# Kernel tuning notes

Hardware: AMD Instinct MI355X
Metric: run time of the kernel (lower is better)

## Reference

```python
import jax, jax.numpy as jnp
import numpy as np

N, S, E = 50000, 16, 400000
D, EDIM = 128, 64
H, K = 4, 32          # n_head, per-head output_dim
NMP, DEPTH = 2, 2


def attn_agg(x, neigh, Wq, Wk, Wv):
    # x: [n, D], neigh: [n, s, D], W*: [H, D, K]
    q = jnp.einsum('nd,hdk->nhk', x, Wq)
    k = jnp.einsum('nsd,hdk->nshk', neigh, Wk)
    v = jnp.einsum('nsd,hdk->nshk', neigh, Wv)
    scale = jnp.asarray(1.0 / np.sqrt(K), x.dtype)
    scores = jnp.einsum('nhk,nshk->nhs', q, k) * scale
    attn = jax.nn.softmax(scores, axis=-1)
    out = jax.nn.elu(jnp.einsum('nhs,nshk->nhk', attn, v))  # activation per head
    return out.reshape(out.shape[0], H * K)                  # concat heads


def setup_inputs():
    key = jax.random.key(0)
    ks = jax.random.split(key, 14)
    sD, sE = 1.0 / np.sqrt(D), 1.0 / np.sqrt(EDIM)
    return {
        'feats': jax.random.normal(ks[0], (N, D), jnp.float32),
        'node_emb': jax.random.normal(ks[1], (N, D), jnp.float32) * 0.02,
        'Wprep': jax.random.normal(ks[2], (D, D), jnp.float32) * sD,
        'edge_emb': jax.random.normal(ks[3], (NMP, E, EDIM), jnp.float32),
        'Wedgeprep': jax.random.normal(ks[4], (NMP, EDIM, D), jnp.float32) * sE,
        'Wq_e': jax.random.normal(ks[5], (NMP, DEPTH, H, D, K), jnp.float32) * sD,
        'Wk_e': jax.random.normal(ks[6], (NMP, DEPTH, H, D, K), jnp.float32) * sD,
        'Wv_e': jax.random.normal(ks[7], (NMP, DEPTH, H, D, K), jnp.float32) * sD,
        'Wq_n': jax.random.normal(ks[8], (NMP, DEPTH, H, D, K), jnp.float32) * sD,
        'Wk_n': jax.random.normal(ks[9], (NMP, DEPTH, H, D, K), jnp.float32) * sD,
        'Wv_n': jax.random.normal(ks[10], (NMP, DEPTH, H, D, K), jnp.float32) * sD,
        'node2edge_idx': jax.random.randint(ks[11], (NMP, N, S), 0, E, jnp.int32),
        'edge_node_adj': jax.random.randint(ks[12], (NMP, E, 2), 0, N, jnp.int32),
    }


def reference(feats, node_emb, Wprep, edge_emb, Wedgeprep,
              Wq_e, Wk_e, Wv_e, Wq_n, Wk_n, Wv_n,
              node2edge_idx, edge_node_adj):
    outputs = []
    for mp in range(NMP):
        f = jax.lax.stop_gradient(feats)           # feats[all_ids].detach()
        dummy_feats = node_emb                      # prep layer_idx=0 (id embedding)
        all_feats = f @ Wprep                       # prep layer_idx=1
        all_edges = edge_emb[mp] @ Wedgeprep[mp]    # edge_prep[mp], shuffle=False
        skip = []
        for l in range(DEPTH):
            # --- edge update: gather 2 endpoint node feats per edge ---
            en = all_feats[edge_node_adj[mp]]       # [E, 2, D]
            next_edges = attn_agg(all_edges, en, Wq_e[mp, l], Wk_e[mp, l], Wv_e[mp, l])
            # --- node update: gather S incident edge feats per node (OLD edges) ---
            x = dummy_feats if l == 0 else all_feats
            ne = all_edges[node2edge_idx[mp]]       # [N, S, D]
            next_feats = attn_agg(x, ne, Wq_n[mp, l], Wk_n[mp, l], Wv_n[mp, l])
            skip.append(next_feats)
            all_feats, all_edges = next_feats, next_edges
        outputs.append(jnp.concatenate(skip, axis=-1))  # [N, DEPTH*H*K]
    return jnp.stack(outputs, axis=0)                   # [NMP, N, DEPTH*H*K]
```

## Files before the change

kernel.cpp:

```cpp
#include <hip/hip_runtime.h>

#define N_NODES 50000
#define S_NEI 16
#define E_EDGES 400000
#define DDIM 128
#define EDIMC 64
#define NMPC 2
#define DEPTHC 2

typedef __attribute__((ext_vector_type(8))) short short8v;
typedef __attribute__((ext_vector_type(4))) float float4v;

__device__ __forceinline__ unsigned short f2bf(float f) {
  unsigned int u = __float_as_uint(f);
  unsigned int r = (u + 0x7fffu + ((u >> 16) & 1u)) >> 16;
  return (unsigned short)r;
}
__device__ __forceinline__ float bf2f(unsigned short h) { return __uint_as_float((unsigned int)h << 16); }
__device__ __forceinline__ float bflo(unsigned int u) { return __uint_as_float(u << 16); }
__device__ __forceinline__ float bfhi(unsigned int u) { return __uint_as_float(u & 0xffff0000u); }

__global__ void build_wt(const float* __restrict__ Wprep, const float* __restrict__ Wedgeprep,
                         const float* __restrict__ Wq_e, const float* __restrict__ Wk_e,
                         const float* __restrict__ Wv_e, const float* __restrict__ Wq_n,
                         const float* __restrict__ Wk_n, const float* __restrict__ Wv_n,
                         unsigned short* __restrict__ WT) {
  int idx = blockIdx.x * 256 + threadIdx.x;
  if (idx >= 27 * 16384) return;
  int slot = idx >> 14, r = idx & 16383;
  float v = 0.f;
  if (slot < 24) {
    int ml = slot / 6, mat = slot % 6;
    int c = r >> 7, d = r & 127;
    int h = c >> 5, kk = c & 31;
    const float* W = (mat == 0) ? Wk_e : (mat == 1) ? Wv_e : (mat == 2) ? Wq_n
                   : (mat == 3) ? Wq_e : (mat == 4) ? Wk_n : Wv_n;
    v = W[(((size_t)ml * 4 + h) * 128 + d) * 32 + kk];
  } else if (slot == 24) {
    int c = r >> 7, d = r & 127;
    v = Wprep[d * 128 + c];
  } else {
    int mp = slot - 25;
    int c = r >> 6, k = r & 63;
    if (c < 128) v = Wedgeprep[((size_t)mp * 64 + k) * 128 + c];
  }
  WT[idx] = f2bf(v);
}

template<int KDIM, int NW, bool ASPLIT>
__global__ __launch_bounds__(256, 3)
void proj(const unsigned short* __restrict__ Xbf, const float* __restrict__ Xf,
          const unsigned short* __restrict__ WT,
          unsigned short* __restrict__ Y0, unsigned short* __restrict__ Y1,
          unsigned short* __restrict__ Y2, int rs0, int rs1, int rs2, int M) {
  constexpr int NKK  = KDIM / 32;
  constexpr int CHPR = KDIM / 8;
  constexpr int SWZ  = CHPR - 1;
  __shared__ unsigned short Wl[128 * KDIM];
  const int tid  = threadIdx.x;
  const int lane = tid & 63;
  const int wv   = tid >> 6;
  const int l15  = lane & 15, lg = lane >> 4;
  const long m0  = (long)blockIdx.x * 128 + wv * 32;

  short8v xb[2][NKK];
  #pragma unroll
  for (int rf = 0; rf < 2; ++rf) {
    long row = m0 + rf * 16 + l15; if (row >= M) row = M - 1;
    #pragma unroll
    for (int kk = 0; kk < NKK; ++kk) {
      const int k0 = kk * 32 + lg * 8;
      if (ASPLIT) {
        const float* p = Xf + row * KDIM + k0;
        float4v a0 = *(const float4v*)p;
        float4v a1 = *(const float4v*)(p + 4);
        #pragma unroll
        for (int j = 0; j < 8; ++j) {
          float x = (j < 4) ? a0[j] : a1[j - 4];
          xb[rf][kk][j] = (short)f2bf(x);
        }
      } else {
        xb[rf][kk] = *(const short8v*)(Xbf + row * KDIM + k0);
      }
    }
  }

  unsigned short* Ys[3] = {Y0, Y1, Y2};
  const int rsv[3] = {rs0, rs1, rs2};
  #pragma unroll
  for (int w = 0; w < NW; ++w) {
    if (w) __syncthreads();
    {
      const uint4* src = (const uint4*)(WT + (size_t)w * 16384);
      #pragma unroll
      for (int i = 0; i < CHPR / 2; ++i) {
        int ci = i * 256 + tid;
        int row = ci / CHPR, ch = ci & SWZ;
        uint4 v = src[ci];
        *(uint4*)((char*)Wl + row * (KDIM * 2) + ((ch ^ (row & SWZ)) << 4)) = v;
      }
    }
    __syncthreads();

    float4v acc[8][2];
    #pragma unroll
    for (int cf = 0; cf < 8; ++cf)
      #pragma unroll
      for (int rf = 0; rf < 2; ++rf) acc[cf][rf] = (float4v)0.f;

    #pragma unroll
    for (int kk = 0; kk < NKK; ++kk) {
      #pragma unroll
      for (int cf = 0; cf < 8; ++cf) {
        const int row = cf * 16 + l15;
        const int ch  = (kk * 4 + lg) ^ (row & SWZ);
        short8v b = *(const short8v*)((char*)Wl + row * (KDIM * 2) + (ch << 4));
        acc[cf][0] = __builtin_amdgcn_mfma_f32_16x16x32_bf16(b, xb[0][kk], acc[cf][0], 0, 0, 0);
        acc[cf][1] = __builtin_amdgcn_mfma_f32_16x16x32_bf16(b, xb[1][kk], acc[cf][1], 0, 0, 0);
      }
    }

    #pragma unroll
    for (int rf = 0; rf < 2; ++rf) {
      const long m = m0 + rf * 16 + l15;
      if (m < M) {
        #pragma unroll
        for (int cf = 0; cf < 8; ++cf) {
          const int c0 = cf * 16 + lg * 4;
          float4v a = acc[cf][rf];
          ushort4 o;
          o.x = f2bf(a[0]); o.y = f2bf(a[1]); o.z = f2bf(a[2]); o.w = f2bf(a[3]);
          *(ushort4*)(Ys[w] + m * (long)rsv[w] + c0) = o;
        }
      }
    }
  }
}

template<int PREP>
__global__ __launch_bounds__(512, 4)
void edge_fused(unsigned short* __restrict__ ehi, const unsigned short* __restrict__ WTqe,
                const unsigned short* __restrict__ KVn, const int* __restrict__ adj,
                unsigned short* __restrict__ KVe,
                const float* __restrict__ emb, const unsigned short* __restrict__ WTprep) {
  __shared__ unsigned short Wl[128 * 128];
  const int tid  = threadIdx.x;
  const int lane = tid & 63;
  const int wv   = tid >> 6;
  const int l15  = lane & 15, lg = lane >> 4;
  const long m0  = (long)blockIdx.x * 128 + wv * 16;

  const long e = m0 + l15;
  const int2 nn = *(const int2*)(adj + e * 2);
  const size_t b0 = (size_t)nn.x * 256, b1 = (size_t)nn.y * 256;

  short8v xb[4];
  if (PREP) {
    {
      const uint4* src = (const uint4*)WTprep;
      #pragma unroll
      for (int i = 0; i < 2; ++i) {
        int ci = i * 512 + tid;
        int row = ci >> 3, ch = ci & 7;
        uint4 v = src[ci];
        *(uint4*)((char*)Wl + row * 128 + ((ch ^ (row & 7)) << 4)) = v;
      }
    }
    short8v eb[2];
    {
      const long row = m0 + l15;
      #pragma unroll
      for (int kk = 0; kk < 2; ++kk) {
        const float* p = emb + row * 64 + kk * 32 + lg * 8;
        float4v a0 = *(const float4v*)p;
        float4v a1 = *(const float4v*)(p + 4);
        #pragma unroll
        for (int j = 0; j < 8; ++j) {
          float x = (j < 4) ? a0[j] : a1[j - 4];
          eb[kk][j] = (short)f2bf(x);
        }
      }
    }
    __syncthreads();
    float4v accP[8];
    #pragma unroll
    for (int cf = 0; cf < 8; ++cf) accP[cf] = (float4v)0.f;
    #pragma unroll
    for (int kk = 0; kk < 2; ++kk) {
      #pragma unroll
      for (int cf = 0; cf < 8; ++cf) {
        const int row = cf * 16 + l15;
        const int ch  = (kk * 4 + lg) ^ (row & 7);
        short8v b = *(const short8v*)((char*)Wl + row * 128 + (ch << 4));
        accP[cf] = __builtin_amdgcn_mfma_f32_16x16x32_bf16(b, eb[kk], accP[cf], 0, 0, 0);
      }
    }
    __syncthreads();
    {
      const int er = wv * 16 + l15;
      #pragma unroll
      for (int cf = 0; cf < 8; ++cf) {
        float4v a = accP[cf];
        ushort4 o;
        o.x = f2bf(a[0]); o.y = f2bf(a[1]); o.z = f2bf(a[2]); o.w = f2bf(a[3]);
        const int ch16 = cf * 2 + (lg >> 1);
        const int off  = er * 256 + ((ch16 ^ (er & 15)) << 4) + (lg & 1) * 8;
        *(ushort4*)((char*)Wl + off) = o;
      }
    }
    __syncthreads();
    {
      const int row = wv * 16 + l15;
      #pragma unroll
      for (int kk = 0; kk < 4; ++kk) {
        const int ch = (kk * 4 + lg) ^ (row & 15);
        xb[kk] = *(const short8v*)((char*)Wl + row * 256 + (ch << 4));
      }
    }
  } else {
    const long row = m0 + l15;
    #pragma unroll
    for (int kk = 0; kk < 4; ++kk)
      xb[kk] = *(const short8v*)(ehi + row * 128 + kk * 32 + lg * 8);
  }

  float4v accQ[8];
  ushort4 gk0[8], gk1[8];
  const int slot_of[3] = {1, 2, 0};
  #pragma unroll
  for (int ph = 0; ph < 3; ++ph) {
    if (ph || PREP) __syncthreads();
    {
      const uint4* src = (const uint4*)(WTqe + (size_t)slot_of[ph] * 16384);
      #pragma unroll
      for (int i = 0; i < 4; ++i) {
        int ci = i * 512 + tid;
        int row = ci >> 4, ch = ci & 15;
        uint4 v = src[ci];
        *(uint4*)((char*)Wl + row * 256 + ((ch ^ (row & 15)) << 4)) = v;
      }
    }
    __syncthreads();

    if (ph == 2) {
      #pragma unroll
      for (int cf = 0; cf < 8; ++cf) {
        const int c0 = cf * 16 + lg * 4;
        gk0[cf] = *(const ushort4*)(KVn + b0 + c0);
        gk1[cf] = *(const ushort4*)(KVn + b1 + c0);
      }
    }

    float4v acc[8];
    #pragma unroll
    for (int cf = 0; cf < 8; ++cf) acc[cf] = (float4v)0.f;

    #pragma unroll
    for (int kk = 0; kk < 4; ++kk) {
      #pragma unroll
      for (int cf = 0; cf < 8; ++cf) {
        const int row = cf * 16 + l15;
        const int ch  = (kk * 4 + lg) ^ (row & 15);
        short8v b = *(const short8v*)((char*)Wl + row * 256 + (ch << 4));
        acc[cf] = __builtin_amdgcn_mfma_f32_16x16x32_bf16(b, xb[kk], acc[cf], 0, 0, 0);
      }
    }

    if (ph < 2) {
      const long m = m0 + l15;
      #pragma unroll
      for (int cf = 0; cf < 8; ++cf) {
        const int c0 = cf * 16 + lg * 4;
        float4v a = acc[cf];
        ushort4 o;
        o.x = f2bf(a[0]); o.y = f2bf(a[1]); o.z = f2bf(a[2]); o.w = f2bf(a[3]);
        *(ushort4*)(KVe + m * 256 + ph * 128 + c0) = o;
      }
    } else {
      #pragma unroll
      for (int cf = 0; cf < 8; ++cf) accQ[cf] = acc[cf];
    }
  }

  const float scale = 0.17677669529663687f;
  {
    float p0[4] = {0.f, 0.f, 0.f, 0.f}, p1[4] = {0.f, 0.f, 0.f, 0.f};
    #pragma unroll
    for (int cf = 0; cf < 8; ++cf) {
      const int h = cf >> 1;
      ushort4 k0 = gk0[cf];
      ushort4 k1 = gk1[cf];
      float4v q = accQ[cf];
      p0[h] += q[0] * bf2f(k0.x) + q[1] * bf2f(k0.y) + q[2] * bf2f(k0.z) + q[3] * bf2f(k0.w);
      p1[h] += q[0] * bf2f(k1.x) + q[1] * bf2f(k1.y) + q[2] * bf2f(k1.z) + q[3] * bf2f(k1.w);
    }
    float a0[4], a1[4];
    #pragma unroll
    for (int h = 0; h < 4; ++h) {
      p0[h] += __shfl_xor(p0[h], 16); p0[h] += __shfl_xor(p0[h], 32);
      p1[h] += __shfl_xor(p1[h], 16); p1[h] += __shfl_xor(p1[h], 32);
      const float s0 = p0[h] * scale, s1 = p1[h] * scale;
      const float mx = fmaxf(s0, s1);
      const float e0 = __expf(s0 - mx), e1 = __expf(s1 - mx);
      const float inv = 1.0f / (e0 + e1);
      a0[h] = e0 * inv; a1[h] = e1 * inv;
    }
    #pragma unroll
    for (int cf = 0; cf < 8; ++cf) {
      const int c0 = cf * 16 + lg * 4;
      const int h = cf >> 1;
      ushort4 v0 = *(const ushort4*)(KVn + b0 + 128 + c0);
      ushort4 v1 = *(const ushort4*)(KVn + b1 + 128 + c0);
      float o[4];
      o[0] = a0[h] * bf2f(v0.x) + a1[h] * bf2f(v1.x);
      o[1] = a0[h] * bf2f(v0.y) + a1[h] * bf2f(v1.y);
      o[2] = a0[h] * bf2f(v0.z) + a1[h] * bf2f(v1.z);
      o[3] = a0[h] * bf2f(v0.w) + a1[h] * bf2f(v1.w);
      o[0] = o[0] > 0.f ? o[0] : expm1f(o[0]);
      o[1] = o[1] > 0.f ? o[1] : expm1f(o[1]);
      o[2] = o[2] > 0.f ? o[2] : expm1f(o[2]);
      o[3] = o[3] > 0.f ? o[3] : expm1f(o[3]);
      ushort4 ob;
      ob.x = f2bf(o[0]); ob.y = f2bf(o[1]); ob.z = f2bf(o[2]); ob.w = f2bf(o[3]);
      *(ushort4*)(ehi + e * 128 + c0) = ob;
    }
  }
}

__global__ __launch_bounds__(256)
void node_attn(const unsigned int* __restrict__ Qn, const unsigned int* __restrict__ KVe,
               const int* __restrict__ n2e,
               unsigned short* __restrict__ fhi, float* __restrict__ outp) {
  const int lane = threadIdx.x & 63;
  const long n = (long)blockIdx.x * 4 + (threadIdx.x >> 6);
  const unsigned int q = Qn[n * 64 + lane];
  unsigned int kk[16], vv[16];
  #pragma unroll
  for (int s = 0; s < 16; ++s) {
    const long e = n2e[n * 16 + s];
    kk[s] = KVe[e * 128 + lane];
    vv[s] = KVe[e * 128 + 64 + lane];
  }
  const float qa = bflo(q), qb = bfhi(q);
  float sc[16];
  #pragma unroll
  for (int s = 0; s < 16; ++s) {
    float p = qa * bflo(kk[s]) + qb * bfhi(kk[s]);
    #pragma unroll
    for (int off = 1; off < 16; off <<= 1) p += __shfl_xor(p, off);
    sc[s] = p * 0.17677669529663687f;
  }
  float m = sc[0];
  #pragma unroll
  for (int s = 1; s < 16; ++s) m = fmaxf(m, sc[s]);
  float sum = 0.f;
  #pragma unroll
  for (int s = 0; s < 16; ++s) { sc[s] = __expf(sc[s] - m); sum += sc[s]; }
  const float inv = 1.0f / sum;
  float oa = 0.f, ob = 0.f;
  #pragma unroll
  for (int s = 0; s < 16; ++s) { oa += sc[s] * bflo(vv[s]); ob += sc[s] * bfhi(vv[s]); }
  oa *= inv; ob *= inv;
  oa = oa > 0.f ? oa : expm1f(oa);
  ob = ob > 0.f ? ob : expm1f(ob);
  ((unsigned int*)fhi)[n * 64 + lane] = (unsigned int)f2bf(oa) | ((unsigned int)f2bf(ob) << 16);
  *(float2*)(outp + n * 256 + lane * 2) = make_float2(oa, ob);
}

extern "C" void kernel_launch(void* const* d_in, const int* in_sizes, int n_in,
                              void* d_out, int out_size, void* d_ws, size_t ws_size,
                              hipStream_t stream) {
  const float* feats     = (const float*)d_in[0];
  const float* node_emb  = (const float*)d_in[1];
  const float* Wprep     = (const float*)d_in[2];
  const float* edge_emb  = (const float*)d_in[3];
  const float* Wedgeprep = (const float*)d_in[4];
  const float* Wq_e      = (const float*)d_in[5];
  const float* Wk_e      = (const float*)d_in[6];
  const float* Wv_e      = (const float*)d_in[7];
  const float* Wq_n      = (const float*)d_in[8];
  const float* Wk_n      = (const float*)d_in[9];
  const float* Wv_n      = (const float*)d_in[10];
  const int*   n2e       = (const int*)d_in[11];
  const int*   adj       = (const int*)d_in[12];
  float* out = (float*)d_out;

  char* w = (char*)d_ws;
  auto carve = [&](size_t bytes) -> char* {
    char* p = w; w += (bytes + 255) & ~(size_t)255; return p;
  };
  unsigned short* ehi   = (unsigned short*)carve((size_t)E_EDGES * 128 * 2);
  unsigned short* fprep = (unsigned short*)carve((size_t)N_NODES * 128 * 2);
  unsigned short* fa    = (unsigned short*)carve((size_t)N_NODES * 128 * 2);
  unsigned short* fb    = (unsigned short*)carve((size_t)N_NODES * 128 * 2);
  unsigned short* KVe   = (unsigned short*)carve((size_t)E_EDGES * 256 * 2);
  unsigned short* KVn   = (unsigned short*)carve((size_t)N_NODES * 256 * 2);
  unsigned short* Qn    = (unsigned short*)carve((size_t)N_NODES * 128 * 2);
  unsigned short* WT    = (unsigned short*)carve((size_t)27 * 16384 * 2);

  build_wt<<<(27 * 16384 + 255) / 256, 256, 0, stream>>>(
      Wprep, Wedgeprep, Wq_e, Wk_e, Wv_e, Wq_n, Wk_n, Wv_n, WT);

  const int gN = (N_NODES + 127) / 128;
  const int gE = E_EDGES / 128;

  proj<128, 1, true><<<gN, 256, 0, stream>>>(
      nullptr, feats, WT + (size_t)24 * 16384, fprep, nullptr, nullptr, 128, 0, 0, N_NODES);

  for (int mp = 0; mp < NMPC; ++mp) {
    unsigned short *fchi = fprep, *fnhi = fa;
    for (int l = 0; l < DEPTHC; ++l) {
      const int ml = mp * 2 + l;
      const unsigned short* base = WT + (size_t)ml * 6 * 16384;
      if (l == 0) {
        proj<128, 2, false><<<gN, 256, 0, stream>>>(
            fchi, nullptr, base, KVn, KVn + 128, nullptr, 256, 256, 0, N_NODES);
        proj<128, 1, true><<<gN, 256, 0, stream>>>(
            nullptr, node_emb, base + (size_t)2 * 16384, Qn, nullptr, nullptr, 128, 0, 0, N_NODES);
        edge_fused<1><<<gE, 512, 0, stream>>>(
            ehi, base + (size_t)3 * 16384, KVn, adj + (size_t)mp * E_EDGES * 2, KVe,
            edge_emb + (size_t)mp * E_EDGES * EDIMC, WT + (size_t)(25 + mp) * 16384);
      } else {
        proj<128, 3, false><<<gN, 256, 0, stream>>>(
            fchi, nullptr, base, KVn, KVn + 128, Qn, 256, 256, 128, N_NODES);
        edge_fused<0><<<gE, 512, 0, stream>>>(
            ehi, base + (size_t)3 * 16384, KVn, adj + (size_t)mp * E_EDGES * 2, KVe,
            nullptr, nullptr);
      }
      node_attn<<<N_NODES / 4, 256, 0, stream>>>(
          (const unsigned int*)Qn, (const unsigned int*)KVe,
          n2e + (size_t)mp * N_NODES * S_NEI, fnhi,
          out + (size_t)mp * N_NODES * 256 + (size_t)l * 128);

      fchi = fnhi; fnhi = fb;
    }
  }
}
```

Before: 1.212 ms.

## Fold node-side K/V projections into query via Wq·Wkᵀ and post-aggregation V projection

After: 1.238 ms. 2.1% more time.

```diff
diff --git a/kernel.cpp b/kernel.cpp
--- a/kernel.cpp
+++ b/kernel.cpp
@@ -17,8 +17,7 @@
   return (unsigned short)r;
 }
 __device__ __forceinline__ float bf2f(unsigned short h) { return __uint_as_float((unsigned int)h << 16); }
-__device__ __forceinline__ float bflo(unsigned int u) { return __uint_as_float(u << 16); }
-__device__ __forceinline__ float bfhi(unsigned int u) { return __uint_as_float(u & 0xffff0000u); }
+__device__ __forceinline__ float bfs(short h) { return bf2f((unsigned short)h); }
 
 __global__ void build_wt(const float* __restrict__ Wprep, const float* __restrict__ Wedgeprep,
                          const float* __restrict__ Wq_e, const float* __restrict__ Wk_e,
@@ -47,12 +46,34 @@
   WT[idx] = f2bf(v);
 }
 
+__global__ void build_qk(const float* __restrict__ Wq_n, const float* __restrict__ Wk_n,
+                         unsigned short* __restrict__ QT) {
+  int idx = blockIdx.x * 256 + threadIdx.x;
+  int mh = idx >> 14, r = idx & 16383;
+  int cp = r >> 7, d = r & 127;
+  const float* q = Wq_n + ((size_t)mh * 128 + d) * 32;
+  const float* k = Wk_n + ((size_t)mh * 128 + cp) * 32;
+  float s = 0.f;
+  #pragma unroll
+  for (int j = 0; j < 32; ++j) s += q[j] * k[j];
+  QT[idx] = f2bf(s);
+}
+
+__global__ void build_wv(const float* __restrict__ Wv_n, unsigned short* __restrict__ WV) {
+  int idx = blockIdx.x * 256 + threadIdx.x;
+  int ml = idx >> 14, r14 = idx & 16383;
+  int r = r14 >> 7, d = r14 & 127;
+  int h = r >> 5, kp = r & 31;
+  WV[idx] = f2bf(Wv_n[(((size_t)ml * 4 + h) * 128 + d) * 32 + kp]);
+}
+
 template<int KDIM, int NW, bool ASPLIT>
 __global__ __launch_bounds__(256, 3)
 void proj(const unsigned short* __restrict__ Xbf, const float* __restrict__ Xf,
           const unsigned short* __restrict__ WT,
           unsigned short* __restrict__ Y0, unsigned short* __restrict__ Y1,
-          unsigned short* __restrict__ Y2, int rs0, int rs1, int rs2, int M) {
+          unsigned short* __restrict__ Y2, unsigned short* __restrict__ Y3,
+          int rs0, int rs1, int rs2, int rs3, int M) {
   constexpr int NKK  = KDIM / 32;
   constexpr int CHPR = KDIM / 8;
   constexpr int SWZ  = CHPR - 1;
@@ -85,8 +106,8 @@
     }
   }
 
-  unsigned short* Ys[3] = {Y0, Y1, Y2};
-  const int rsv[3] = {rs0, rs1, rs2};
+  unsigned short* Ys[4] = {Y0, Y1, Y2, Y3};
+  const int rsv[4] = {rs0, rs1, rs2, rs3};
   #pragma unroll
   for (int w = 0; w < NW; ++w) {
     if (w) __syncthreads();
@@ -139,9 +160,9 @@
 
 template<int PREP>
 __global__ __launch_bounds__(512, 4)
-void edge_fused(unsigned short* __restrict__ ehi, const unsigned short* __restrict__ WTqe,
+void edge_fused(unsigned short* __restrict__ eold, const unsigned short* __restrict__ WTq,
                 const unsigned short* __restrict__ KVn, const int* __restrict__ adj,
-                unsigned short* __restrict__ KVe,
+                unsigned short* __restrict__ enew,
                 const float* __restrict__ emb, const unsigned short* __restrict__ WTprep) {
   __shared__ unsigned short Wl[128 * 128];
   const int tid  = threadIdx.x;
@@ -210,6 +231,16 @@
     }
     __syncthreads();
     {
+      unsigned short* dst = eold + (size_t)blockIdx.x * 16384;
+      #pragma unroll
+      for (int i = 0; i < 4; ++i) {
+        int c = i * 512 + tid;
+        int row = c >> 4, ch = c & 15;
+        uint4 v = *(const uint4*)((char*)Wl + row * 256 + ((ch ^ (row & 15)) << 4));
+        *(uint4*)(dst + (size_t)c * 8) = v;
+      }
+    }
+    {
       const int row = wv * 16 + l15;
       #pragma unroll
       for (int kk = 0; kk < 4; ++kk) {
@@ -217,68 +248,45 @@
         xb[kk] = *(const short8v*)((char*)Wl + row * 256 + (ch << 4));
       }
     }
+    __syncthreads();
   } else {
     const long row = m0 + l15;
     #pragma unroll
     for (int kk = 0; kk < 4; ++kk)
-      xb[kk] = *(const short8v*)(ehi + row * 128 + kk * 32 + lg * 8);
+      xb[kk] = *(const short8v*)(eold + row * 128 + kk * 32 + lg * 8);
+  }
+
+  {
+    const uint4* src = (const uint4*)WTq;
+    #pragma unroll
+    for (int i = 0; i < 4; ++i) {
+      int ci = i * 512 + tid;
+      int row = ci >> 4, ch = ci & 15;
+      uint4 v = src[ci];
+      *(uint4*)((char*)Wl + row * 256 + ((ch ^ (row & 15)) << 4)) = v;
+    }
+  }
+  __syncthreads();
+
+  ushort4 gk0[8], gk1[8];
+  #pragma unroll
+  for (int cf = 0; cf < 8; ++cf) {
+    const int c0 = cf * 16 + lg * 4;
+    gk0[cf] = *(const ushort4*)(KVn + b0 + c0);
+    gk1[cf] = *(const ushort4*)(KVn + b1 + c0);
   }
 
   float4v accQ[8];
-  ushort4 gk0[8], gk1[8];
-  const int slot_of[3] = {1, 2, 0};
-  #pragma unroll
-  for (int ph = 0; ph < 3; ++ph) {
-    if (ph || PREP) __syncthreads();
-    {
-      const uint4* src = (const uint4*)(WTqe + (size_t)slot_of[ph] * 16384);
-      #pragma unroll
-      for (int i = 0; i < 4; ++i) {
-        int ci = i * 512 + tid;
-        int row = ci >> 4, ch = ci & 15;
-        uint4 v = src[ci];
-        *(uint4*)((char*)Wl + row * 256 + ((ch ^ (row & 15)) << 4)) = v;
-      }
-    }
-    __syncthreads();
-
-    if (ph == 2) {
-      #pragma unroll
-      for (int cf = 0; cf < 8; ++cf) {
-        const int c0 = cf * 16 + lg * 4;
-        gk0[cf] = *(const ushort4*)(KVn + b0 + c0);
-        gk1[cf] = *(const ushort4*)(KVn + b1 + c0);
-      }
-    }
-
-    float4v acc[8];
-    #pragma unroll
-    for (int cf = 0; cf < 8; ++cf) acc[cf] = (float4v)0.f;
-
-    #pragma unroll
-    for (int kk = 0; kk < 4; ++kk) {
-      #pragma unroll
-      for (int cf = 0; cf < 8; ++cf) {
-        const int row = cf * 16 + l15;
-        const int ch  = (kk * 4 + lg) ^ (row & 15);
-        short8v b = *(const short8v*)((char*)Wl + row * 256 + (ch << 4));
-        acc[cf] = __builtin_amdgcn_mfma_f32_16x16x32_bf16(b, xb[kk], acc[cf], 0, 0, 0);
-      }
-    }
-
-    if (ph < 2) {
-      const long m = m0 + l15;
-      #pragma unroll
-      for (int cf = 0; cf < 8; ++cf) {
-        const int c0 = cf * 16 + lg * 4;
-        float4v a = acc[cf];
-        ushort4 o;
-        o.x = f2bf(a[0]); o.y = f2bf(a[1]); o.z = f2bf(a[2]); o.w = f2bf(a[3]);
-        *(ushort4*)(KVe + m * 256 + ph * 128 + c0) = o;
-      }
-    } else {
-      #pragma unroll
-      for (int cf = 0; cf < 8; ++cf) accQ[cf] = acc[cf];
+  #pragma unroll
+  for (int cf = 0; cf < 8; ++cf) accQ[cf] = (float4v)0.f;
+  #pragma unroll
+  for (int kk = 0; kk < 4; ++kk) {
+    #pragma unroll
+    for (int cf = 0; cf < 8; ++cf) {
+      const int row = cf * 16 + l15;
+      const int ch  = (kk * 4 + lg) ^ (row & 15);
+      short8v b = *(const short8v*)((char*)Wl + row * 256 + (ch << 4));
+      accQ[cf] = __builtin_amdgcn_mfma_f32_16x16x32_bf16(b, xb[kk], accQ[cf], 0, 0, 0);
     }
   }
 
@@ -322,32 +330,32 @@
       o[3] = o[3] > 0.f ? o[3] : expm1f(o[3]);
       ushort4 ob;
       ob.x = f2bf(o[0]); ob.y = f2bf(o[1]); ob.z = f2bf(o[2]); ob.w = f2bf(o[3]);
-      *(ushort4*)(ehi + e * 128 + c0) = ob;
-    }
-  }
-}
-
-__global__ __launch_bounds__(256)
-void node_attn(const unsigned int* __restrict__ Qn, const unsigned int* __restrict__ KVe,
-               const int* __restrict__ n2e,
-               unsigned short* __restrict__ fhi, float* __restrict__ outp) {
+      *(ushort4*)(enew + e * 128 + c0) = ob;
+    }
+  }
+}
+
+__global__ __launch_bounds__(256, 2)
+void node_attn(const unsigned short* __restrict__ qt, const unsigned short* __restrict__ eold,
+               const int* __restrict__ n2e, unsigned short* __restrict__ Z) {
   const int lane = threadIdx.x & 63;
   const long n = (long)blockIdx.x * 4 + (threadIdx.x >> 6);
-  const unsigned int q = Qn[n * 64 + lane];
-  unsigned int kk[16], vv[16];
+  const short8v qv = *(const short8v*)(qt + n * 512 + lane * 8);
+  const int i8 = (lane & 15) * 8;
+  short8v xk[16];
   #pragma unroll
   for (int s = 0; s < 16; ++s) {
     const long e = n2e[n * 16 + s];
-    kk[s] = KVe[e * 128 + lane];
-    vv[s] = KVe[e * 128 + 64 + lane];
-  }
-  const float qa = bflo(q), qb = bfhi(q);
+    xk[s] = *(const short8v*)(eold + e * 128 + i8);
+  }
   float sc[16];
   #pragma unroll
   for (int s = 0; s < 16; ++s) {
-    float p = qa * bflo(kk[s]) + qb * bfhi(kk[s]);
-    #pragma unroll
-    for (int off = 1; off < 16; off <<= 1) p += __shfl_xor(p, off);
+    float p = 0.f;
+    #pragma unroll
+    for (int j = 0; j < 8; ++j) p += bfs(qv[j]) * bfs(xk[s][j]);
+    p += __shfl_xor(p, 1); p += __shfl_xor(p, 2);
+    p += __shfl_xor(p, 4); p += __shfl_xor(p, 8);
     sc[s] = p * 0.17677669529663687f;
   }
   float m = sc[0];
@@ -357,14 +365,83 @@
   #pragma unroll
   for (int s = 0; s < 16; ++s) { sc[s] = __expf(sc[s] - m); sum += sc[s]; }
   const float inv = 1.0f / sum;
-  float oa = 0.f, ob = 0.f;
-  #pragma unroll
-  for (int s = 0; s < 16; ++s) { oa += sc[s] * bflo(vv[s]); ob += sc[s] * bfhi(vv[s]); }
-  oa *= inv; ob *= inv;
-  oa = oa > 0.f ? oa : expm1f(oa);
-  ob = ob > 0.f ? ob : expm1f(ob);
-  ((unsigned int*)fhi)[n * 64 + lane] = (unsigned int)f2bf(oa) | ((unsigned int)f2bf(ob) << 16);
-  *(float2*)(outp + n * 256 + lane * 2) = make_float2(oa, ob);
+  float z[8] = {0.f, 0.f, 0.f, 0.f, 0.f, 0.f, 0.f, 0.f};
+  #pragma unroll
+  for (int s = 0; s < 16; ++s)
+    #pragma unroll
+    for (int j = 0; j < 8; ++j) z[j] += sc[s] * bfs(xk[s][j]);
+  ushort4 o0, o1;
+  o0.x = f2bf(z[0] * inv); o0.y = f2bf(z[1] * inv); o0.z = f2bf(z[2] * inv); o0.w = f2bf(z[3] * inv);
+  o1.x = f2bf(z[4] * inv); o1.y = f2bf(z[5] * inv); o1.z = f2bf(z[6] * inv); o1.w = f2bf(z[7] * inv);
+  *(ushort4*)(Z + n * 512 + lane * 8) = o0;
+  *(ushort4*)(Z + n * 512 + lane * 8 + 4) = o1;
+}
+
+__global__ __launch_bounds__(256, 2)
+void node_post(const unsigned short* __restrict__ Zb, const unsigned short* __restrict__ WV,
+               unsigned short* __restrict__ fnext, float* __restrict__ outp, int M) {
+  __shared__ unsigned short Wl[128 * 128];
+  const int tid  = threadIdx.x;
+  const int lane = tid & 63;
+  const int wv   = tid >> 6;
+  const int l15  = lane & 15, lg = lane >> 4;
+  const long m0  = (long)blockIdx.x * 128 + wv * 32;
+  {
+    const uint4* src = (const uint4*)WV;
+    #pragma unroll
+    for (int i = 0; i < 8; ++i) {
+      int ci = i * 256 + tid;
+      int row = ci >> 4, ch = ci & 15;
+      uint4 v = src[ci];
+      *(uint4*)((char*)Wl + row * 256 + ((ch ^ (row & 15)) << 4)) = v;
+    }
+  }
+  __syncthreads();
+
+  #pragma unroll
+  for (int h = 0; h < 4; ++h) {
+    float4v acc[2][2];
+    #pragma unroll
+    for (int cf = 0; cf < 2; ++cf)
+      #pragma unroll
+      for (int rf = 0; rf < 2; ++rf) acc[cf][rf] = (float4v)0.f;
+    #pragma unroll
+    for (int rf = 0; rf < 2; ++rf) {
+      long row = m0 + rf * 16 + l15; if (row >= M) row = M - 1;
+      #pragma unroll
+      for (int kk = 0; kk < 4; ++kk) {
+        short8v zb = *(const short8v*)(Zb + row * 512 + h * 128 + kk * 32 + lg * 8);
+        #pragma unroll
+        for (int cf = 0; cf < 2; ++cf) {
+          const int arow = h * 32 + cf * 16 + l15;
+          const int ch = (kk * 4 + lg) ^ (arow & 15);
+          short8v b = *(const short8v*)((char*)Wl + arow * 256 + (ch << 4));
+          acc[cf][rf] = __builtin_amdgcn_mfma_f32_16x16x32_bf16(b, zb, acc[cf][rf], 0, 0, 0);
+        }
+      }
+    }
+    #pragma unroll
+    for (int rf = 0; rf < 2; ++rf) {
+      const long m = m0 + rf * 16 + l15;
+      if (m < M) {
+        #pragma unroll
+        for (int cf = 0; cf < 2; ++cf) {
+          const int c0 = h * 32 + cf * 16 + lg * 4;
+          float o[4];
+          #pragma unroll
+          for (int j = 0; j < 4; ++j) {
+            float a = acc[cf][rf][j];
+            o[j] = a > 0.f ? a : expm1f(a);
+          }
+          ushort4 ob;
+          ob.x = f2bf(o[0]); ob.y = f2bf(o[1]); ob.z = f2bf(o[2]); ob.w = f2bf(o[3]);
+          *(ushort4*)(fnext + m * 128 + c0) = ob;
+          float4 of; of.x = o[0]; of.y = o[1]; of.z = o[2]; of.w = o[3];
+          *(float4*)(outp + m * 256 + c0) = of;
+        }
+      }
+    }
+  }
 }
 
 extern "C" void kernel_launch(void* const* d_in, const int* in_sizes, int n_in,
@@ -389,49 +466,65 @@
   auto carve = [&](size_t bytes) -> char* {
     char* p = w; w += (bytes + 255) & ~(size_t)255; return p;
   };
-  unsigned short* ehi   = (unsigned short*)carve((size_t)E_EDGES * 128 * 2);
+  unsigned short* e_a   = (unsigned short*)carve((size_t)E_EDGES * 128 * 2);
+  unsigned short* e_b   = (unsigned short*)carve((size_t)E_EDGES * 128 * 2);
   unsigned short* fprep = (unsigned short*)carve((size_t)N_NODES * 128 * 2);
   unsigned short* fa    = (unsigned short*)carve((size_t)N_NODES * 128 * 2);
   unsigned short* fb    = (unsigned short*)carve((size_t)N_NODES * 128 * 2);
-  unsigned short* KVe   = (unsigned short*)carve((size_t)E_EDGES * 256 * 2);
   unsigned short* KVn   = (unsigned short*)carve((size_t)N_NODES * 256 * 2);
-  unsigned short* Qn    = (unsigned short*)carve((size_t)N_NODES * 128 * 2);
+  unsigned short* qt    = (unsigned short*)carve((size_t)N_NODES * 512 * 2);
+  unsigned short* Zb    = (unsigned short*)carve((size_t)N_NODES * 512 * 2);
   unsigned short* WT    = (unsigned short*)carve((size_t)27 * 16384 * 2);
+  unsigned short* QT    = (unsigned short*)carve((size_t)16 * 16384 * 2);
+  unsigned short* WV    = (unsigned short*)carve((size_t)4 * 16384 * 2);
 
   build_wt<<<(27 * 16384 + 255) / 256, 256, 0, stream>>>(
       Wprep, Wedgeprep, Wq_e, Wk_e, Wv_e, Wq_n, Wk_n, Wv_n, WT);
+  build_qk<<<16 * 64, 256, 0, stream>>>(Wq_n, Wk_n, QT);
+  build_wv<<<4 * 64, 256, 0, stream>>>(Wv_n, WV);
 
   const int gN = (N_NODES + 127) / 128;
   const int gE = E_EDGES / 128;
 
   proj<128, 1, true><<<gN, 256, 0, stream>>>(
-      nullptr, feats, WT + (size_t)24 * 16384, fprep, nullptr, nullptr, 128, 0, 0, N_NODES);
+      nullptr, feats, WT + (size_t)24 * 16384, fprep, nullptr, nullptr, nullptr,
+      128, 0, 0, 0, N_NODES);
 
   for (int mp = 0; mp < NMPC; ++mp) {
+    unsigned short *ecur = e_a, *enext = e_b;
     unsigned short *fchi = fprep, *fnhi = fa;
     for (int l = 0; l < DEPTHC; ++l) {
       const int ml = mp * 2 + l;
       const unsigned short* base = WT + (size_t)ml * 6 * 16384;
+      const unsigned short* qkb  = QT + (size_t)ml * 4 * 16384;
+      proj<128, 2, false><<<gN, 256, 0, stream>>>(
+          fchi, nullptr, base, KVn, KVn + 128, nullptr, nullptr,
+          256, 256, 0, 0, N_NODES);
       if (l == 0) {
-        proj<128, 2, false><<<gN, 256, 0, stream>>>(
-            fchi, nullptr, base, KVn, KVn + 128, nullptr, 256, 256, 0, N_NODES);
-        proj<128, 1, true><<<gN, 256, 0, stream>>>(
-            nullptr, node_emb, base + (size_t)2 * 16384, Qn, nullptr, nullptr, 128, 0, 0, N_NODES);
+        proj<128, 4, true><<<gN, 256, 0, stream>>>(
+            nullptr, node_emb, qkb, qt, qt + 128, qt + 256, qt + 384,
+            512, 512, 512, 512, N_NODES);
+      } else {
+        proj<128, 4, false><<<gN, 256, 0, stream>>>(
+            fchi, nullptr, qkb, qt, qt + 128, qt + 256, qt + 384,
+            512, 512, 512, 512, N_NODES);
+      }
+      if (l == 0) {
         edge_fused<1><<<gE, 512, 0, stream>>>(
-            ehi, base + (size_t)3 * 16384, KVn, adj + (size_t)mp * E_EDGES * 2, KVe,
+            ecur, base + (size_t)3 * 16384, KVn, adj + (size_t)mp * E_EDGES * 2, enext,
             edge_emb + (size_t)mp * E_EDGES * EDIMC, WT + (size_t)(25 + mp) * 16384);
       } else {
-        proj<128, 3, false><<<gN, 256, 0, stream>>>(
-            fchi, nullptr, base, KVn, KVn + 128, Qn, 256, 256, 128, N_NODES);
         edge_fused<0><<<gE, 512, 0, stream>>>(
-            ehi, base + (size_t)3 * 16384, KVn, adj + (size_t)mp * E_EDGES * 2, KVe,
+            ecur, base + (size_t)3 * 16384, KVn, adj + (size_t)mp * E_EDGES * 2, enext,
             nullptr, nullptr);
       }
       node_attn<<<N_NODES / 4, 256, 0, stream>>>(
-          (const unsigned int*)Qn, (const unsigned int*)KVe,
-          n2e + (size_t)mp * N_NODES * S_NEI, fnhi,
-          out + (size_t)mp * N_NODES * 256 + (size_t)l * 128);
-
+          qt, ecur, n2e + (size_t)mp * N_NODES * S_NEI, Zb);
+      node_post<<<gN, 256, 0, stream>>>(
+          Zb, WV + (size_t)ml * 16384, fnhi,
+          out + (size_t)mp * N_NODES * 256 + (size_t)l * 128, N_NODES);
+
+      unsigned short* t = ecur; ecur = enext; enext = t;
       fchi = fnhi; fnhi = fb;
     }
   }
```
